# Performance work log

Measured on AMD Instinct MI355X. Metric: run time of the kernel, lower is better.

The kernel has to match this reference:

```python
import jax, jax.numpy as jnp
import numpy as np

D_MODEL = 512
H = 8
C = 2


def setup_inputs() -> dict:
    key = jax.random.key(0)
    kq, kk, kv = jax.random.split(key, 3)
    B, L = 16, 1024
    Q = jax.random.normal(kq, (B, L, D_MODEL), dtype=jnp.float32)
    K = jax.random.normal(kk, (B, L, D_MODEL), dtype=jnp.float32)
    V = jax.random.normal(kv, (B, L, D_MODEL), dtype=jnp.float32)
    return {"Q": Q, "K": K, "V": V}


def reference(Q, K, V):
    B, L, dm = Q.shape
    d = dm // H
    # [B, h, L, d]
    q = Q.reshape(B, L, H, d).transpose(0, 2, 1, 3)
    k = K.reshape(B, L, H, d).transpose(0, 2, 1, 3)
    v = V.reshape(B, L, H, d).transpose(0, 2, 1, 3)

    # auto-correlation via FFT along the time axis (axis=2)
    qf = jnp.fft.fft(q, axis=2)
    kf = jnp.fft.fft(k, axis=2)
    corr = jnp.fft.ifft(qf * jnp.conj(kf), axis=2).real.astype(Q.dtype)  # [B,h,L,d]

    topk = int(C * np.log(L))  # static
    # top-k over the lag axis (L); lax.top_k works on last axis
    w, idx = jax.lax.top_k(corr.transpose(0, 1, 3, 2), topk)  # [B,h,d,k]
    w = jax.nn.softmax(w, axis=-1)
    w = w.transpose(0, 1, 3, 2)      # [B,h,k,d]
    idx = idx.transpose(0, 1, 3, 2)  # [B,h,k,d]

    # time-delay aggregation: out[t] = sum_i w_i * v[min(idx_i + t, L-1)]
    t = jnp.arange(L)
    gidx = jnp.minimum(idx[:, :, :, None, :] + t[None, None, None, :, None], L - 1)  # [B,h,k,L,d]
    gathered = jnp.take_along_axis(v[:, :, None, :, :], gidx, axis=3)  # [B,h,k,L,d]
    out = jnp.einsum('bhkd,bhkld->bhld', w, gathered)  # [B,h,L,d]

    return out.transpose(0, 2, 1, 3).reshape(B, L, dm)
```

## Files before the change

kernel.cpp:

```cpp
#include <hip/hip_runtime.h>
#include <float.h>

#define LSEQ 1024
#define NCH  8192
#define TOPK 13

typedef short bf16x8 __attribute__((ext_vector_type(8)));
typedef float f32x16 __attribute__((ext_vector_type(16)));

#define CH_BYTES 12416

__device__ __forceinline__ unsigned swzA(unsigned a) {
  return a ^ ((a >> 3) & 48u) ^ ((a >> 1) & 32u);
}
__device__ __forceinline__ unsigned packhi(unsigned hi, unsigned lo) {
  return __builtin_amdgcn_perm(hi, lo, 0x07060302u);
}
__device__ __forceinline__ float resid(float x) {
  return x - __uint_as_float(__float_as_uint(x) & 0xffff0000u);
}
__device__ __forceinline__ f32x16 mfma_bf16(bf16x8 a, bf16x8 b, f32x16 c) {
  return __builtin_amdgcn_mfma_f32_32x32x16_bf16(a, b, c, 0, 0, 0);
}

__global__ __launch_bounds__(256) void pack_qk(const float* __restrict__ Qg,
                                               const float* __restrict__ Kg,
                                               unsigned char* __restrict__ kpack,
                                               unsigned char* __restrict__ qpack) {
  __shared__ float tile[32][33];
  int zz = blockIdx.z;
  const float* src = (zz < 16 ? Qg : Kg) + (size_t)(zz & 15) * 1024 * 512;
  int t0 = blockIdx.y * 32, c0 = blockIdx.x * 32;
  int tx = threadIdx.x, ty = threadIdx.y;
#pragma unroll
  for (int j = 0; j < 32; j += 8)
    tile[ty + j][tx] = src[(size_t)(t0 + ty + j) * 512 + (c0 + tx)];
  __syncthreads();
  int cg = (zz & 15) * 512 + c0 + tx;
  int e0 = 4 * ty;
  float f0 = tile[e0][tx], f1 = tile[e0 + 1][tx];
  float f2 = tile[e0 + 2][tx], f3 = tile[e0 + 3][tx];
  unsigned h0 = packhi(__float_as_uint(f1), __float_as_uint(f0));
  unsigned h1 = packhi(__float_as_uint(f3), __float_as_uint(f2));
  unsigned l0 = packhi(__float_as_uint(resid(f1)), __float_as_uint(resid(f0)));
  unsigned l1 = packhi(__float_as_uint(resid(f3)), __float_as_uint(resid(f2)));
  if (zz < 16) {
    *(uint4*)(qpack + (size_t)cg * 4096 + 4 * (t0 + e0)) = make_uint4(h0, l0, h1, l1);
  } else {
    unsigned a = swzA((unsigned)(2 * (t0 + e0)));
    *(uint2*)(kpack + (size_t)cg * 4096 + a)        = make_uint2(h0, h1);
    *(uint2*)(kpack + (size_t)cg * 4096 + 2048 + a) = make_uint2(l0, l1);
  }
}

__global__ __launch_bounds__(256) void corr_fused_kernel(const unsigned char* __restrict__ qpack,
                                                         const unsigned char* __restrict__ kpack,
                                                         const float* __restrict__ Vg,
                                                         float* __restrict__ outg) {
  __shared__ __align__(16) unsigned char lds_raw[4 * CH_BYTES];
  const int tid = threadIdx.x, wave = tid >> 6, lane = tid & 63;
  const int bid = blockIdx.x;
  const int cblk = (bid & 7) * 256 + (bid >> 3);
  const int cg0 = cblk * 4;
  const int b = cg0 >> 9, col0 = cg0 & 511;
  const int c = cg0 + wave;
  unsigned char* myc = lds_raw + wave * CH_BYTES;

  {
    const uint4* ks = (const uint4*)(kpack + (size_t)c * 4096);
    const uint4* qs = (const uint4*)(qpack + (size_t)c * 4096);
    uint4* kd = (uint4*)myc;
    uint4* qd = (uint4*)(myc + 4096);
#pragma unroll
    for (int it = 0; it < 4; ++it) {
      kd[lane + 64 * it] = ks[lane + 64 * it];
      qd[lane + 64 * it] = qs[lane + 64 * it];
    }
    if (lane < 2) qd[256 + lane] = qs[lane];
  }

  {
    unsigned* qe = (unsigned*)(myc + 4096);
    unsigned* qo = (unsigned*)(myc + 8256);
    uint4 r0 = *(const uint4*)(qe + 16 * lane);
    uint4 r1 = *(const uint4*)(qe + 16 * lane + 4);
    uint4 r2 = *(const uint4*)(qe + 16 * lane + 8);
    uint4 r3 = *(const uint4*)(qe + 16 * lane + 12);
    uint2 r4 = *(const uint2*)(qe + 16 * lane + 16);
    unsigned h9[9] = {r0.x, r0.z, r1.x, r1.z, r2.x, r2.z, r3.x, r3.z, r4.x};
    unsigned l9[9] = {r0.y, r0.w, r1.y, r1.w, r2.y, r2.w, r3.y, r3.w, r4.y};
    unsigned o16[16];
#pragma unroll
    for (int i = 0; i < 8; ++i) {
      o16[2 * i]     = __builtin_amdgcn_alignbyte(h9[i + 1], h9[i], 2);
      o16[2 * i + 1] = __builtin_amdgcn_alignbyte(l9[i + 1], l9[i], 2);
    }
    *(uint4*)(qo + 16 * lane)      = make_uint4(o16[0],  o16[1],  o16[2],  o16[3]);
    *(uint4*)(qo + 16 * lane + 4)  = make_uint4(o16[4],  o16[5],  o16[6],  o16[7]);
    *(uint4*)(qo + 16 * lane + 8)  = make_uint4(o16[8],  o16[9],  o16[10], o16[11]);
    *(uint4*)(qo + 16 * lane + 12) = make_uint4(o16[12], o16[13], o16[14], o16[15]);
    if (lane == 0) {
      *(uint4*)(qo + 1024) = make_uint4(o16[0], o16[1], o16[2], o16[3]);
      *(uint4*)(qo + 1028) = make_uint4(o16[4], o16[5], o16[6], o16[7]);
    }
  }

  const int row = lane & 31, Hh = lane >> 5;
  const int rp  = 2 * (row & 15) + (row >> 4);
  unsigned e0   = (unsigned)((8 * Hh - rp) & 1023);
  const int par = rp & 1;
  const unsigned char* bArr = myc + (par ? 8256 : 4096);
  unsigned boff = (((par ? (e0 - 1) : e0) >> 1) * 8u);
  unsigned tb   = (unsigned)(64 * row + 16 * Hh);

  f32x16 d = {};
#pragma unroll 4
  for (int ks = 0; ks < 64; ++ks) {
    unsigned sa = swzA(tb);
    uint4 Ah = *(const uint4*)(myc + sa);
    uint4 Al = *(const uint4*)(myc + 2048 + sa);
    uint2 p0 = *(const uint2*)(bArr + boff);
    uint2 p1 = *(const uint2*)(bArr + boff + 8);
    uint2 p2 = *(const uint2*)(bArr + boff + 16);
    uint2 p3 = *(const uint2*)(bArr + boff + 24);
    bf16x8 fah = __builtin_bit_cast(bf16x8, Ah);
    bf16x8 fal = __builtin_bit_cast(bf16x8, Al);
    bf16x8 fbh = __builtin_bit_cast(bf16x8, make_uint4(p0.x, p1.x, p2.x, p3.x));
    bf16x8 fbl = __builtin_bit_cast(bf16x8, make_uint4(p0.y, p1.y, p2.y, p3.y));
    d = mfma_bf16(fah, fbh, d);
    d = mfma_bf16(fal, fbh, d);
    d = mfma_bf16(fah, fbl, d);
    tb   = (tb + 32u) & 2047u;
    boff = (boff + 64u) & 4095u;
  }

  float acc[16];
#pragma unroll
  for (int i = 0; i < 16; ++i) acc[i] = d[i];
  const int ibase = 128 * Hh + rp;

  float topv[TOPK]; int topi[TOPK];
  for (int r = 0; r < TOPK; ++r) {
    float m = -FLT_MAX; int mi = 0x7fffffff;
#pragma unroll
    for (int j = 0; j < 16; ++j) {
      int idx = ibase + 32 * ((j & 3) + 8 * (j >> 2));
      if (acc[j] > m || (acc[j] == m && idx < mi)) { m = acc[j]; mi = idx; }
    }
#pragma unroll
    for (int offx = 32; offx >= 1; offx >>= 1) {
      float om = __shfl_xor(m, offx);
      int   oi = __shfl_xor(mi, offx);
      if (om > m || (om == m && oi < mi)) { m = om; mi = oi; }
    }
    topv[r] = m; topi[r] = mi;
#pragma unroll
    for (int j = 0; j < 16; ++j)
      acc[j] = (ibase + 32 * ((j & 3) + 8 * (j >> 2)) == mi) ? -FLT_MAX : acc[j];
  }
  float mx = topv[0];
  float w[TOPK]; float wsum = 0.f;
#pragma unroll
  for (int r = 0; r < TOPK; ++r) { w[r] = __expf(topv[r] - mx); wsum += w[r]; }
  float inv = 1.0f / wsum;
  int di[TOPK];
#pragma unroll
  for (int r = 0; r < TOPK; ++r) { w[r] *= inv; di[r] = (1024 - topi[r]) & 1023; }

  __syncthreads();
  {
    const float* Vb = Vg + ((size_t)b * 1024) * 512 + col0;
#pragma unroll
    for (int j = 0; j < 4; ++j) {
      int t = tid + 256 * j;
      float4 vv = *(const float4*)(Vb + (size_t)t * 512);
      ((float*)(lds_raw + 0 * CH_BYTES))[t] = vv.x;
      ((float*)(lds_raw + 1 * CH_BYTES))[t] = vv.y;
      ((float*)(lds_raw + 2 * CH_BYTES))[t] = vv.z;
      ((float*)(lds_raw + 3 * CH_BYTES))[t] = vv.w;
    }
  }
  __syncthreads();

  {
    const float* vls = (const float*)myc;
    float* obuf = (float*)(myc + 8256);
#pragma unroll 4
    for (int j = 0; j < 16; ++j) {
      int t = lane + 64 * j;
      float a = 0.f;
#pragma unroll
      for (int i = 0; i < TOPK; ++i) {
        int src = di[i] + t; src = src < 1023 ? src : 1023;
        a += w[i] * vls[src];
      }
      obuf[t] = a;
    }
  }
  __syncthreads();

  {
    float* o = outg + ((size_t)b * 1024) * 512 + col0;
#pragma unroll
    for (int jj = 0; jj < 4; ++jj) {
      int t = tid + 256 * jj;
      float4 ov;
      ov.x = ((const float*)(lds_raw + 0 * CH_BYTES + 8256))[t];
      ov.y = ((const float*)(lds_raw + 1 * CH_BYTES + 8256))[t];
      ov.z = ((const float*)(lds_raw + 2 * CH_BYTES + 8256))[t];
      ov.w = ((const float*)(lds_raw + 3 * CH_BYTES + 8256))[t];
      *(float4*)(o + (size_t)t * 512) = ov;
    }
  }
}

extern "C" void kernel_launch(void* const* d_in, const int* in_sizes, int n_in,
                              void* d_out, int out_size, void* d_ws, size_t ws_size,
                              hipStream_t stream) {
  const float* Q = (const float*)d_in[0];
  const float* K = (const float*)d_in[1];
  const float* V = (const float*)d_in[2];
  float* out = (float*)d_out;
  unsigned char* kpack = (unsigned char*)d_ws;
  unsigned char* qpack = kpack + (size_t)NCH * 4096;

  dim3 tb(32, 8);
  pack_qk<<<dim3(16, 32, 32), tb, 0, stream>>>(Q, K, kpack, qpack);
  corr_fused_kernel<<<NCH / 4, 256, 0, stream>>>(qpack, kpack, V, out);
}
```

Before: 246.8 us.

## Fuse Q/K bf16 split packing into the correlation kernel, dropping the pack pass

Removes the separate pack_qk kernel and its workspace round trip. Each block now reads its four Q/K columns straight from global memory as float4, splits each value into hi/lo bf16 parts, and writes them into the swizzled LDS layout the MFMA loop expects. This saves one kernel launch and a full write plus read of the packed buffers. In exchange the global loads are strided 16-byte reads, and the LDS writes are many scattered 2-byte stores.

```diff
diff --git a/kernel.cpp b/kernel.cpp
--- a/kernel.cpp
+++ b/kernel.cpp
@@ -13,9 +13,6 @@
 __device__ __forceinline__ unsigned swzA(unsigned a) {
   return a ^ ((a >> 3) & 48u) ^ ((a >> 1) & 32u);
 }
-__device__ __forceinline__ unsigned packhi(unsigned hi, unsigned lo) {
-  return __builtin_amdgcn_perm(hi, lo, 0x07060302u);
-}
 __device__ __forceinline__ float resid(float x) {
   return x - __uint_as_float(__float_as_uint(x) & 0xffff0000u);
 }
@@ -23,40 +20,10 @@
   return __builtin_amdgcn_mfma_f32_32x32x16_bf16(a, b, c, 0, 0, 0);
 }
 
-__global__ __launch_bounds__(256) void pack_qk(const float* __restrict__ Qg,
-                                               const float* __restrict__ Kg,
-                                               unsigned char* __restrict__ kpack,
-                                               unsigned char* __restrict__ qpack) {
-  __shared__ float tile[32][33];
-  int zz = blockIdx.z;
-  const float* src = (zz < 16 ? Qg : Kg) + (size_t)(zz & 15) * 1024 * 512;
-  int t0 = blockIdx.y * 32, c0 = blockIdx.x * 32;
-  int tx = threadIdx.x, ty = threadIdx.y;
-#pragma unroll
-  for (int j = 0; j < 32; j += 8)
-    tile[ty + j][tx] = src[(size_t)(t0 + ty + j) * 512 + (c0 + tx)];
-  __syncthreads();
-  int cg = (zz & 15) * 512 + c0 + tx;
-  int e0 = 4 * ty;
-  float f0 = tile[e0][tx], f1 = tile[e0 + 1][tx];
-  float f2 = tile[e0 + 2][tx], f3 = tile[e0 + 3][tx];
-  unsigned h0 = packhi(__float_as_uint(f1), __float_as_uint(f0));
-  unsigned h1 = packhi(__float_as_uint(f3), __float_as_uint(f2));
-  unsigned l0 = packhi(__float_as_uint(resid(f1)), __float_as_uint(resid(f0)));
-  unsigned l1 = packhi(__float_as_uint(resid(f3)), __float_as_uint(resid(f2)));
-  if (zz < 16) {
-    *(uint4*)(qpack + (size_t)cg * 4096 + 4 * (t0 + e0)) = make_uint4(h0, l0, h1, l1);
-  } else {
-    unsigned a = swzA((unsigned)(2 * (t0 + e0)));
-    *(uint2*)(kpack + (size_t)cg * 4096 + a)        = make_uint2(h0, h1);
-    *(uint2*)(kpack + (size_t)cg * 4096 + 2048 + a) = make_uint2(l0, l1);
-  }
-}
-
-__global__ __launch_bounds__(256) void corr_fused_kernel(const unsigned char* __restrict__ qpack,
-                                                         const unsigned char* __restrict__ kpack,
-                                                         const float* __restrict__ Vg,
-                                                         float* __restrict__ outg) {
+__global__ __launch_bounds__(256) void corr_mega_kernel(const float* __restrict__ Qg,
+                                                        const float* __restrict__ Kg,
+                                                        const float* __restrict__ Vg,
+                                                        float* __restrict__ outg) {
   __shared__ __align__(16) unsigned char lds_raw[4 * CH_BYTES];
   const int tid = threadIdx.x, wave = tid >> 6, lane = tid & 63;
   const int bid = blockIdx.x;
@@ -64,20 +31,40 @@
   const int cg0 = cblk * 4;
   const int b = cg0 >> 9, col0 = cg0 & 511;
   const int c = cg0 + wave;
+  (void)c;
   unsigned char* myc = lds_raw + wave * CH_BYTES;
 
   {
-    const uint4* ks = (const uint4*)(kpack + (size_t)c * 4096);
-    const uint4* qs = (const uint4*)(qpack + (size_t)c * 4096);
-    uint4* kd = (uint4*)myc;
-    uint4* qd = (uint4*)(myc + 4096);
-#pragma unroll
-    for (int it = 0; it < 4; ++it) {
-      kd[lane + 64 * it] = ks[lane + 64 * it];
-      qd[lane + 64 * it] = qs[lane + 64 * it];
-    }
-    if (lane < 2) qd[256 + lane] = qs[lane];
-  }
+    const float* Qb = Qg + ((size_t)b * 1024) * 512 + col0;
+    const float* Kb = Kg + ((size_t)b * 1024) * 512 + col0;
+#pragma unroll
+    for (int j = 0; j < 4; ++j) {
+      int t = tid + 256 * j;
+      float4 kv = *(const float4*)(Kb + (size_t)t * 512);
+      float4 qv = *(const float4*)(Qb + (size_t)t * 512);
+      unsigned ka0 = swzA(4u * (unsigned)(t >> 1) + 2u * (unsigned)(t & 1));
+      unsigned qa0 = 8u * (unsigned)(t >> 1) + 2u * (unsigned)(t & 1);
+      float karr[4] = {kv.x, kv.y, kv.z, kv.w};
+      float qarr[4] = {qv.x, qv.y, qv.z, qv.w};
+#pragma unroll
+      for (int cc = 0; cc < 4; ++cc) {
+        unsigned char* ck = lds_raw + cc * CH_BYTES;
+        unsigned khiv = __float_as_uint(karr[cc]) >> 16;
+        unsigned klov = __float_as_uint(resid(karr[cc])) >> 16;
+        *(unsigned short*)(ck + ka0)        = (unsigned short)khiv;
+        *(unsigned short*)(ck + 2048 + ka0) = (unsigned short)klov;
+        unsigned qhiv = __float_as_uint(qarr[cc]) >> 16;
+        unsigned qlov = __float_as_uint(resid(qarr[cc])) >> 16;
+        *(unsigned short*)(ck + 4096 + qa0)     = (unsigned short)qhiv;
+        *(unsigned short*)(ck + 4096 + qa0 + 4) = (unsigned short)qlov;
+        if (t < 8) {
+          *(unsigned short*)(ck + 8192 + qa0)     = (unsigned short)qhiv;
+          *(unsigned short*)(ck + 8192 + qa0 + 4) = (unsigned short)qlov;
+        }
+      }
+    }
+  }
+  __syncthreads();
 
   {
     unsigned* qe = (unsigned*)(myc + 4096);
@@ -221,10 +208,7 @@
   const float* K = (const float*)d_in[1];
   const float* V = (const float*)d_in[2];
   float* out = (float*)d_out;
-  unsigned char* kpack = (unsigned char*)d_ws;
-  unsigned char* qpack = kpack + (size_t)NCH * 4096;
-
-  dim3 tb(32, 8);
-  pack_qk<<<dim3(16, 32, 32), tb, 0, stream>>>(Q, K, kpack, qpack);
-  corr_fused_kernel<<<NCH / 4, 256, 0, stream>>>(qpack, kpack, V, out);
-}
+  (void)d_ws; (void)ws_size;
+
+  corr_mega_kernel<<<NCH / 4, 256, 0, stream>>>(Q, K, V, out);
+}
```

Measured after the change: 226.6 us. -8.2%, faster.
